# Optimization experiments

Hardware: AMD Instinct MI355X
Metric: run time of the kernel (lower is better)

Reference implementation:

```python
import jax, jax.numpy as jnp
import numpy as np

MARGIN = 5.0
NUM_CLASSES = 21


def setup_inputs() -> dict:
    key = jax.random.key(0)
    k1, k2, k3 = jax.random.split(key, 3)
    B, D, C = 65536, 512, NUM_CLASSES
    features = jax.random.normal(k1, (B, D), dtype=jnp.float32)
    centers = jax.random.normal(k2, (C, D), dtype=jnp.float32)
    labels = jax.random.randint(k3, (B,), 0, C, dtype=jnp.int64)
    return {"features": features, "centers": centers, "labels": labels}


def reference(features, centers, labels):
    # Halved squared euclidean distances, batch x num_classes, via the
    # ||f||^2 + ||c||^2 - 2 f.c expansion (avoids a B x C x D intermediate).
    f2 = jnp.sum(features * features, axis=1, keepdims=True)      # (B, 1)
    c2 = jnp.sum(centers * centers, axis=1)[None, :]              # (1, C)
    d = 0.5 * (f2 + c2 - 2.0 * (features @ centers.T))            # (B, C)

    B = features.shape[0]
    pos = d[jnp.arange(B), labels]                                 # dist to own center
    same = labels[:, None] == jnp.arange(NUM_CLASSES)[None, :]     # (B, C)
    neg = jnp.min(jnp.where(same, jnp.inf, d), axis=1)             # nearest other center
    loss = jnp.mean(jax.nn.relu(pos + MARGIN - neg))
    return loss
```

## Files before the change

### kernel.cpp

```cpp
#include <hip/hip_runtime.h>
#include <float.h>

#define DIM      512
#define NCLS     21
#define MARGIN_V 5.0f
#define ROWS_PB  64
#define NWAVES   8
#define DSLICE   (DIM / NWAVES)
#define DC       16
#define NSTAGE   (DSLICE / DC)
#define LPAD     (DC + 1)
#define TILEF    (ROWS_PB * LPAD)
#define CLDSF    (NCLS * DIM)
#define CST      (NCLS + 1)

__global__ __launch_bounds__(64)
void center_norm_kernel(const float* __restrict__ centers,
                        float* __restrict__ halfc2) {
    const int c = blockIdx.x;
    const int t = threadIdx.x;
    float s = 0.f;
#pragma unroll
    for (int i = 0; i < DIM / 64; ++i) {
        float v = centers[c * DIM + i * 64 + t];
        s = fmaf(v, v, s);
    }
#pragma unroll
    for (int off = 32; off > 0; off >>= 1)
        s += __shfl_down(s, off, 64);
    if (t == 0) halfc2[c] = 0.5f * s;
}

__global__ __launch_bounds__(512, 4)
void tcl_main_kernel(const float* __restrict__ feat,
                     const float* __restrict__ centers,
                     const int* __restrict__ labels,
                     const float* __restrict__ halfc2,
                     float* __restrict__ out) {
    __shared__ float lds[CLDSF + NWAVES * TILEF];

    const int tid  = threadIdx.x;
    const int w    = __builtin_amdgcn_readfirstlane(tid >> 6);
    const int t    = tid & 63;
    const int row0 = blockIdx.x * ROWS_PB;

    float acc[NCLS];
#pragma unroll
    for (int c = 0; c < NCLS; ++c) acc[c] = 0.f;

    const float4* fbase = reinterpret_cast<const float4*>(feat);
    const int rsub = t >> 2;
    const int j4   = t & 3;
    const size_t gbase = (size_t)(row0 + rsub) * (DIM / 4)
                       + (size_t)w * (DSLICE / 4) + j4;

    float4 pre[4];
#pragma unroll
    for (int i = 0; i < 4; ++i)
        pre[i] = fbase[gbase + (size_t)i * 16 * (DIM / 4)];
    __builtin_amdgcn_sched_barrier(0);

    {
        const float4* c4 = reinterpret_cast<const float4*>(centers);
        float4* l4 = reinterpret_cast<float4*>(lds);
#pragma unroll
        for (int i = 0; i < (CLDSF / 4 + 511) / 512; ++i) {
            int idx = i * 512 + tid;
            if (idx < CLDSF / 4) l4[idx] = c4[idx];
        }
    }

    float* mytile = &lds[CLDSF + w * TILEF];
    const int wbase = rsub * LPAD + j4 * 4;

    __syncthreads();

#pragma unroll 1
    for (int s = 0; s < NSTAGE; ++s) {
#pragma unroll
        for (int i = 0; i < 4; ++i) {
            int b = i * 16 * LPAD + wbase;
            mytile[b + 0] = pre[i].x;
            mytile[b + 1] = pre[i].y;
            mytile[b + 2] = pre[i].z;
            mytile[b + 3] = pre[i].w;
        }
        if (s + 1 < NSTAGE) {
#pragma unroll
            for (int i = 0; i < 4; ++i)
                pre[i] = fbase[gbase + (size_t)i * 16 * (DIM / 4)
                               + (size_t)(s + 1) * (DC / 4)];
        }
        __builtin_amdgcn_sched_barrier(0);

        const int dbase = w * DSLICE + s * DC;
#pragma unroll 2
        for (int jj = 0; jj < DC; jj += 4) {
            float f0 = mytile[t * LPAD + jj + 0];
            float f1 = mytile[t * LPAD + jj + 1];
            float f2 = mytile[t * LPAD + jj + 2];
            float f3 = mytile[t * LPAD + jj + 3];
#pragma unroll
            for (int ch = 0; ch < 3; ++ch) {
                float4 cv[7];
#pragma unroll
                for (int k = 0; k < 7; ++k)
                    cv[k] = *reinterpret_cast<const float4*>(
                        &lds[(ch * 7 + k) * DIM + dbase + jj]);
#pragma unroll
                for (int k = 0; k < 7; ++k) {
                    int c = ch * 7 + k;
                    acc[c] = fmaf(f0, cv[k].x,
                              fmaf(f1, cv[k].y,
                               fmaf(f2, cv[k].z,
                                fmaf(f3, cv[k].w, acc[c]))));
                }
            }
        }
    }

    float* comb = lds;
    __syncthreads();
    if (w >= 4) {
        float* p = &comb[((w - 4) * ROWS_PB + t) * CST];
#pragma unroll
        for (int c = 0; c < NCLS; ++c) p[c] = acc[c];
    }
    __syncthreads();
    if (w < 4) {
        const float* p = &comb[(w * ROWS_PB + t) * CST];
#pragma unroll
        for (int c = 0; c < NCLS; ++c) acc[c] += p[c];
    }
    __syncthreads();
    if (w == 2 || w == 3) {
        float* p = &comb[((w - 2) * ROWS_PB + t) * CST];
#pragma unroll
        for (int c = 0; c < NCLS; ++c) p[c] = acc[c];
    }
    __syncthreads();
    if (w < 2) {
        const float* p = &comb[(w * ROWS_PB + t) * CST];
#pragma unroll
        for (int c = 0; c < NCLS; ++c) acc[c] += p[c];
    }
    __syncthreads();
    if (w == 1) {
        float* p = &comb[t * CST];
#pragma unroll
        for (int c = 0; c < NCLS; ++c) p[c] = acc[c];
    }
    __syncthreads();
    if (w == 0) {
        const float* p = &comb[t * CST];
        const int lab = labels[row0 + t];
        float pos = 0.f, neg = FLT_MAX;
#pragma unroll
        for (int c = 0; c < NCLS; ++c) {
            float e = halfc2[c] - (acc[c] + p[c]);
            pos = (c == lab) ? e : pos;
            neg = (c == lab) ? neg : fminf(neg, e);
        }
        float v = fmaxf(pos + MARGIN_V - neg, 0.f);
#pragma unroll
        for (int off = 32; off > 0; off >>= 1)
            v += __shfl_down(v, off, 64);
        if (t == 0) atomicAdd(out, v * (1.0f / 65536.f));
    }
}

extern "C" void kernel_launch(void* const* d_in, const int* in_sizes, int n_in,
                              void* d_out, int out_size, void* d_ws, size_t ws_size,
                              hipStream_t stream) {
    const float* feat    = (const float*)d_in[0];
    const float* centers = (const float*)d_in[1];
    const int*   labels  = (const int*)d_in[2];
    float* out    = (float*)d_out;
    float* halfc2 = (float*)d_ws;

    hipMemsetAsync(d_out, 0, (size_t)out_size * sizeof(float), stream);
    center_norm_kernel<<<NCLS, 64, 0, stream>>>(centers, halfc2);

    const int nblocks = 65536 / ROWS_PB;
    tcl_main_kernel<<<nblocks, 512, 0, stream>>>(feat, centers, labels, halfc2, out);
}
```

Baseline: 204.6 us.

## Register-block four rows per lane to reuse center LDS loads

```diff
diff --git a/kernel.cpp b/kernel.cpp
--- a/kernel.cpp
+++ b/kernel.cpp
@@ -4,15 +4,16 @@
 #define DIM      512
 #define NCLS     21
 #define MARGIN_V 5.0f
-#define ROWS_PB  64
 #define NWAVES   8
 #define DSLICE   (DIM / NWAVES)
-#define DC       16
+#define RPL      4
+#define ROWS_PB  (64 * RPL)
+#define DC       8
 #define NSTAGE   (DSLICE / DC)
-#define LPAD     (DC + 1)
-#define TILEF    (ROWS_PB * LPAD)
 #define CLDSF    (NCLS * DIM)
-#define CST      (NCLS + 1)
+#define TILEF    (ROWS_PB * DC)
+#define LDSF     (CLDSF + NWAVES * TILEF)
+#define SST      (RPL * NCLS + 1)
 
 __global__ __launch_bounds__(64)
 void center_norm_kernel(const float* __restrict__ centers,
@@ -31,33 +32,33 @@
     if (t == 0) halfc2[c] = 0.5f * s;
 }
 
-__global__ __launch_bounds__(512, 4)
+__global__ __launch_bounds__(512, 2)
 void tcl_main_kernel(const float* __restrict__ feat,
                      const float* __restrict__ centers,
                      const int* __restrict__ labels,
                      const float* __restrict__ halfc2,
                      float* __restrict__ out) {
-    __shared__ float lds[CLDSF + NWAVES * TILEF];
+    __shared__ float lds[LDSF];
 
     const int tid  = threadIdx.x;
     const int w    = __builtin_amdgcn_readfirstlane(tid >> 6);
     const int t    = tid & 63;
     const int row0 = blockIdx.x * ROWS_PB;
 
-    float acc[NCLS];
-#pragma unroll
-    for (int c = 0; c < NCLS; ++c) acc[c] = 0.f;
+    float acc[RPL][NCLS];
+#pragma unroll
+    for (int r = 0; r < RPL; ++r)
+#pragma unroll
+        for (int c = 0; c < NCLS; ++c) acc[r][c] = 0.f;
 
     const float4* fbase = reinterpret_cast<const float4*>(feat);
-    const int rsub = t >> 2;
-    const int j4   = t & 3;
-    const size_t gbase = (size_t)(row0 + rsub) * (DIM / 4)
-                       + (size_t)w * (DSLICE / 4) + j4;
-
-    float4 pre[4];
-#pragma unroll
-    for (int i = 0; i < 4; ++i)
-        pre[i] = fbase[gbase + (size_t)i * 16 * (DIM / 4)];
+    float4 pre[8];
+#pragma unroll
+    for (int i = 0; i < 8; ++i) {
+        int f = i * 64 + t;
+        pre[i] = fbase[(size_t)(row0 + (f >> 1)) * (DIM / 4)
+                       + (size_t)w * (DSLICE / 4) + (f & 1)];
+    }
     __builtin_amdgcn_sched_barrier(0);
 
     {
@@ -71,101 +72,119 @@
     }
 
     float* mytile = &lds[CLDSF + w * TILEF];
-    const int wbase = rsub * LPAD + j4 * 4;
 
     __syncthreads();
 
 #pragma unroll 1
     for (int s = 0; s < NSTAGE; ++s) {
 #pragma unroll
-        for (int i = 0; i < 4; ++i) {
-            int b = i * 16 * LPAD + wbase;
-            mytile[b + 0] = pre[i].x;
-            mytile[b + 1] = pre[i].y;
-            mytile[b + 2] = pre[i].z;
-            mytile[b + 3] = pre[i].w;
+        for (int i = 0; i < 8; ++i) {
+            int f = i * 64 + t;
+            *reinterpret_cast<float4*>(
+                &mytile[(f & 1) * (ROWS_PB * 4) + (f >> 1) * 4]) = pre[i];
         }
         if (s + 1 < NSTAGE) {
 #pragma unroll
-            for (int i = 0; i < 4; ++i)
-                pre[i] = fbase[gbase + (size_t)i * 16 * (DIM / 4)
-                               + (size_t)(s + 1) * (DC / 4)];
+            for (int i = 0; i < 8; ++i) {
+                int f = i * 64 + t;
+                pre[i] = fbase[(size_t)(row0 + (f >> 1)) * (DIM / 4)
+                               + (size_t)w * (DSLICE / 4)
+                               + (size_t)(s + 1) * (DC / 4) + (f & 1)];
+            }
         }
         __builtin_amdgcn_sched_barrier(0);
 
-        const int dbase = w * DSLICE + s * DC;
-#pragma unroll 2
-        for (int jj = 0; jj < DC; jj += 4) {
-            float f0 = mytile[t * LPAD + jj + 0];
-            float f1 = mytile[t * LPAD + jj + 1];
-            float f2 = mytile[t * LPAD + jj + 2];
-            float f3 = mytile[t * LPAD + jj + 3];
+#pragma unroll
+        for (int j2 = 0; j2 < 2; ++j2) {
+            float4 fv[RPL];
+#pragma unroll
+            for (int r = 0; r < RPL; ++r)
+                fv[r] = *reinterpret_cast<const float4*>(
+                    &mytile[j2 * (ROWS_PB * 4) + (t + r * 64) * 4]);
+            const int dbase = w * DSLICE + s * DC + j2 * 4;
 #pragma unroll
             for (int ch = 0; ch < 3; ++ch) {
                 float4 cv[7];
 #pragma unroll
                 for (int k = 0; k < 7; ++k)
                     cv[k] = *reinterpret_cast<const float4*>(
-                        &lds[(ch * 7 + k) * DIM + dbase + jj]);
+                        &lds[(ch * 7 + k) * DIM + dbase]);
 #pragma unroll
                 for (int k = 0; k < 7; ++k) {
-                    int c = ch * 7 + k;
-                    acc[c] = fmaf(f0, cv[k].x,
-                              fmaf(f1, cv[k].y,
-                               fmaf(f2, cv[k].z,
-                                fmaf(f3, cv[k].w, acc[c]))));
+                    const int c = ch * 7 + k;
+#pragma unroll
+                    for (int r = 0; r < RPL; ++r) {
+                        acc[r][c] = fmaf(fv[r].x, cv[k].x,
+                                     fmaf(fv[r].y, cv[k].y,
+                                      fmaf(fv[r].z, cv[k].z,
+                                       fmaf(fv[r].w, cv[k].w, acc[r][c]))));
+                    }
                 }
             }
         }
     }
 
-    float* comb = lds;
+    float* scratch = lds;
     __syncthreads();
     if (w >= 4) {
-        float* p = &comb[((w - 4) * ROWS_PB + t) * CST];
-#pragma unroll
-        for (int c = 0; c < NCLS; ++c) p[c] = acc[c];
+        float* p = &scratch[((w - 4) * 64 + t) * SST];
+#pragma unroll
+        for (int r = 0; r < RPL; ++r)
+#pragma unroll
+            for (int c = 0; c < NCLS; ++c) p[r * NCLS + c] = acc[r][c];
     }
     __syncthreads();
     if (w < 4) {
-        const float* p = &comb[(w * ROWS_PB + t) * CST];
-#pragma unroll
-        for (int c = 0; c < NCLS; ++c) acc[c] += p[c];
+        const float* p = &scratch[(w * 64 + t) * SST];
+#pragma unroll
+        for (int r = 0; r < RPL; ++r)
+#pragma unroll
+            for (int c = 0; c < NCLS; ++c) acc[r][c] += p[r * NCLS + c];
     }
     __syncthreads();
     if (w == 2 || w == 3) {
-        float* p = &comb[((w - 2) * ROWS_PB + t) * CST];
-#pragma unroll
-        for (int c = 0; c < NCLS; ++c) p[c] = acc[c];
+        float* p = &scratch[((w - 2) * 64 + t) * SST];
+#pragma unroll
+        for (int r = 0; r < RPL; ++r)
+#pragma unroll
+            for (int c = 0; c < NCLS; ++c) p[r * NCLS + c] = acc[r][c];
     }
     __syncthreads();
     if (w < 2) {
-        const float* p = &comb[(w * ROWS_PB + t) * CST];
-#pragma unroll
-        for (int c = 0; c < NCLS; ++c) acc[c] += p[c];
+        const float* p = &scratch[(w * 64 + t) * SST];
+#pragma unroll
+        for (int r = 0; r < RPL; ++r)
+#pragma unroll
+            for (int c = 0; c < NCLS; ++c) acc[r][c] += p[r * NCLS + c];
     }
     __syncthreads();
     if (w == 1) {
-        float* p = &comb[t * CST];
-#pragma unroll
-        for (int c = 0; c < NCLS; ++c) p[c] = acc[c];
+        float* p = &scratch[t * SST];
+#pragma unroll
+        for (int r = 0; r < RPL; ++r)
+#pragma unroll
+            for (int c = 0; c < NCLS; ++c) p[r * NCLS + c] = acc[r][c];
     }
     __syncthreads();
     if (w == 0) {
-        const float* p = &comb[t * CST];
-        const int lab = labels[row0 + t];
-        float pos = 0.f, neg = FLT_MAX;
-#pragma unroll
-        for (int c = 0; c < NCLS; ++c) {
-            float e = halfc2[c] - (acc[c] + p[c]);
-            pos = (c == lab) ? e : pos;
-            neg = (c == lab) ? neg : fminf(neg, e);
-        }
-        float v = fmaxf(pos + MARGIN_V - neg, 0.f);
+        const float* p = &scratch[t * SST];
+        float vsum = 0.f;
+#pragma unroll
+        for (int r = 0; r < RPL; ++r) {
+            const int lab = labels[row0 + t + r * 64];
+            float pos = 0.f, neg = FLT_MAX;
+#pragma unroll
+            for (int c = 0; c < NCLS; ++c) {
+                float e = halfc2[c] - (acc[r][c] + p[r * NCLS + c]);
+                pos = (c == lab) ? e : pos;
+                neg = (c == lab) ? neg : fminf(neg, e);
+            }
+            vsum += fmaxf(pos + MARGIN_V - neg, 0.f);
+        }
 #pragma unroll
         for (int off = 32; off > 0; off >>= 1)
-            v += __shfl_down(v, off, 64);
-        if (t == 0) atomicAdd(out, v * (1.0f / 65536.f));
+            vsum += __shfl_down(vsum, off, 64);
+        if (t == 0) atomicAdd(out, vsum * (1.0f / 65536.f));
     }
 }
 
```

Result: slower. 667.4 us (+226.2%).
